# Kernel optimization log

Measured on AMD Instinct MI355X. Metric: run time of the kernel, lower is better.

Reference implementation:

```python
import jax, jax.numpy as jnp
import numpy as np

N, F_NODE, F_FLOW, H, E, B, L = 131072, 64, 16, 128, 2097152, 256, 32


def setup_inputs() -> dict:
    key = jax.random.key(0)
    ks = jax.random.split(key, 24)
    gn = lambda k, s, sc: jax.random.normal(k, s, jnp.float32) * sc
    s_in = 1.0 / np.sqrt(F_NODE)
    s_h = 1.0 / np.sqrt(H)
    s_f = 1.0 / np.sqrt(F_FLOW)
    s_c = 1.0 / np.sqrt(2 * H + H // 2)
    inp = {
        "x": gn(ks[0], (N, F_NODE), 1.0),
        "edge_index": jax.random.randint(ks[1], (2, E), 0, N),
        "batch": jnp.sort(jax.random.randint(ks[2], (N,), 0, B)),
        "path_idx": jax.random.randint(ks[3], (B, L), 0, N),
        "path_len": jax.random.randint(ks[4], (B,), 1, L + 1),
        "flow": gn(ks[5], (B, F_FLOW), 1.0),
        # SAGEConv1: out = mean_agg(x_j) @ Wl.T + b + x_i @ Wr.T
        "Wl1": gn(ks[6], (H, F_NODE), s_in), "Wr1": gn(ks[7], (H, F_NODE), s_in), "b1": gn(ks[8], (H,), s_in),
        "Wl2": gn(ks[9], (H, H), s_h), "Wr2": gn(ks[10], (H, H), s_h), "b2": gn(ks[11], (H,), s_h),
        # LSTM (torch gate order i,f,g,o)
        "Wih": gn(ks[12], (4 * H, H), s_h), "Whh": gn(ks[13], (4 * H, H), s_h),
        "bih": gn(ks[14], (4 * H,), s_h), "bhh": gn(ks[15], (4 * H,), s_h),
        # flow encoder Linear(F_FLOW, H//2)
        "Wf": gn(ks[16], (H // 2, F_FLOW), s_f), "bf": gn(ks[17], (H // 2,), s_f),
        # scorer MLP: Linear(2H+H//2, H) -> ReLU -> Linear(H, 1)
        "Ws1": gn(ks[18], (H, 2 * H + H // 2), s_c), "bs1": gn(ks[19], (H,), s_c),
        "Ws2": gn(ks[20], (1, H), s_h), "bs2": gn(ks[21], (1,), s_h),
    }
    return inp


def _sage(x, src, dst, Wl, Wr, b, n):
    agg = jax.ops.segment_sum(x[src], dst, num_segments=n)  # [n, d]
    cnt = jax.ops.segment_sum(jnp.ones((src.shape[0],), x.dtype), dst, num_segments=n)
    mean = agg / jnp.maximum(cnt, 1.0)[:, None]
    return mean @ Wl.T + b + x @ Wr.T


def _lstm_final_h(seq, valid, Wih, Whh, bih, bhh):
    # seq: [B, L, H], valid: [B, L] bool; returns h at each path's last valid step
    b, l, h = seq.shape
    h0 = jnp.zeros((b, h), seq.dtype)

    def step(carry, inp):
        hp, cp = carry
        x_t, v = inp  # [B,H], [B]
        gates = x_t @ Wih.T + hp @ Whh.T + bih + bhh
        i, f, g, o = jnp.split(gates, 4, axis=-1)
        c_new = jax.nn.sigmoid(f) * cp + jax.nn.sigmoid(i) * jnp.tanh(g)
        h_new = jax.nn.sigmoid(o) * jnp.tanh(c_new)
        m = v[:, None]
        return (jnp.where(m, h_new, hp), jnp.where(m, c_new, cp)), None

    (hf, _), _ = jax.lax.scan(step, (h0, h0),
                              (jnp.swapaxes(seq, 0, 1), jnp.swapaxes(valid, 0, 1)))
    return hf


def reference(x, edge_index, batch, path_idx, path_len, flow,
              Wl1, Wr1, b1, Wl2, Wr2, b2,
              Wih, Whh, bih, bhh, Wf, bf, Ws1, bs1, Ws2, bs2):
    n = x.shape[0]
    src, dst = edge_index[0], edge_index[1]
    h1 = jax.nn.relu(_sage(x, src, dst, Wl1, Wr1, b1, n))
    node_emb = jax.nn.relu(_sage(h1, src, dst, Wl2, Wr2, b2, n))

    # global mean pool per graph
    gsum = jax.ops.segment_sum(node_emb, batch, num_segments=B)
    gcnt = jax.ops.segment_sum(jnp.ones((n,), node_emb.dtype), batch, num_segments=B)
    graph_emb = gsum / jnp.maximum(gcnt, 1.0)[:, None]  # [B, H]

    flow_emb = jax.nn.relu(flow @ Wf.T + bf)  # [B, H//2]

    path_seq = node_emb[path_idx]  # [B, L, H]
    valid = jnp.arange(L)[None, :] < path_len[:, None]  # [B, L]
    path_emb = _lstm_final_h(path_seq, valid, Wih, Whh, bih, bhh)  # [B, H]

    combined = jnp.concatenate([graph_emb, path_emb, flow_emb], axis=-1)
    hidden = jax.nn.relu(combined @ Ws1.T + bs1)
    scores = hidden @ Ws2.T + bs2  # [B, 1]
    return scores[:, 0]  # matches torch.cat of per-path [1] outputs -> [B]
```

## Files before the change

### kernel.cpp

```cpp
#include <hip/hip_runtime.h>
#include <hip/hip_bf16.h>

#define N_NODES 131072
#define N_EDGES 2097152
#define BATCHES 256
#define LPATH   32
#define NB   256
#define NPB  512
#define GB   256
#define EPB  8192

typedef __hip_bfloat16 bf16;
using short8  = __attribute__((ext_vector_type(8))) short;
using floatx4 = __attribute__((ext_vector_type(4))) float;
using floatx2 = __attribute__((ext_vector_type(2))) float;

__device__ __forceinline__ float bl(unsigned u){ union {unsigned x; float f;} c; c.x = u << 16; return c.f; }
__device__ __forceinline__ float bh(unsigned u){ union {unsigned x; float f;} c; c.x = u & 0xffff0000u; return c.f; }
__device__ __forceinline__ unsigned packbf(float lo, float hi){
  bf16 l = __float2bfloat16(lo), h = __float2bfloat16(hi);
  unsigned short lu, hu;
  __builtin_memcpy(&lu, &l, 2); __builtin_memcpy(&hu, &h, 2);
  return (unsigned)lu | ((unsigned)hu << 16);
}
__device__ __forceinline__ float frcp(float x){ return __builtin_amdgcn_rcpf(x); }
__device__ __forceinline__ float sigf(float x){ return frcp(1.f + __expf(-x)); }
__device__ __forceinline__ float tanh_fast(float x){ return fmaf(2.f, frcp(1.f + __expf(-2.f * x)), -1.f); }

__global__ void mega0_k(const float* __restrict__ x, unsigned* __restrict__ xb8, bf16* __restrict__ Acat1,
                        const int* __restrict__ dst, int* __restrict__ cntA,
                        const float* __restrict__ Wl1, const float* __restrict__ Wr1,
                        const float* __restrict__ Wl2, const float* __restrict__ Wr2,
                        const float* __restrict__ Wih, const float* __restrict__ Whh,
                        const float* __restrict__ bih, const float* __restrict__ bhh,
                        bf16* __restrict__ Wcat1, bf16* __restrict__ Wcat2,
                        bf16* __restrict__ WihB, bf16* __restrict__ WhhB, float* __restrict__ bsumF,
                        const int* __restrict__ batch, int* __restrict__ starts){
  __shared__ int h[NB];
  int bid = blockIdx.x, tid = threadIdx.x;
  if (bid < 8192){
    int g = bid * 256 + tid;
    int n = g >> 4, p = g & 15;
    float4 v = *(const float4*)(x + (size_t)n * 64 + p * 4);
    uint2 wb; wb.x = packbf(v.x, v.y); wb.y = packbf(v.z, v.w);
    *(uint2*)(Acat1 + (size_t)n * 128 + 64 + p * 4) = wb;
    int w = 0;
    w = __builtin_amdgcn_cvt_pk_fp8_f32(v.x, v.y, w, false);
    w = __builtin_amdgcn_cvt_pk_fp8_f32(v.z, v.w, w, true);
    xb8[(size_t)n * 16 + p] = (unsigned)w;
  } else if (bid < 8448){
    int cb = bid - 8192;
    h[tid] = 0;
    __syncthreads();
    int base = cb * EPB;
    #pragma unroll
    for (int i = 0; i < EPB / 256; ++i){
      int d = dst[base + i * 256 + tid];
      atomicAdd(&h[d >> 9], 1);
    }
    __syncthreads();
    cntA[tid * GB + cb] = h[tid];
  } else if (bid < 9155){
    int g = (bid - 8448) * 256 + tid;
    if (g < 16384) {
      int hh = g >> 7, k = g & 127;
      float v = (k < 64) ? Wl1[hh * 64 + k] : Wr1[hh * 64 + (k - 64)];
      Wcat1[g] = __float2bfloat16(v);
    } else if (g < 49152) {
      int q = g - 16384;
      int hh = q >> 8, k = q & 255;
      float v = (k < 128) ? Wl2[hh * 128 + k] : Wr2[hh * 128 + (k - 128)];
      Wcat2[q] = __float2bfloat16(v);
    } else if (g < 114688) {
      int q = g - 49152;
      WihB[q] = __float2bfloat16(Wih[q]);
    } else if (g < 180224) {
      int q = g - 114688;
      WhhB[q] = __float2bfloat16(Whh[q]);
    } else if (g < 180736) {
      int k = g - 180224;
      bsumF[k] = bih[k] + bhh[k];
    }
  } else {
    int b = tid;
    int lo = 0, hi = N_NODES;
    while (lo < hi){ int mid = (lo + hi) >> 1; if (batch[mid] < b) lo = mid + 1; else hi = mid; }
    starts[b] = lo;
    if (b == 0) starts[BATCHES] = N_NODES;
  }
}

__global__ void scan1_k(const int* __restrict__ cnt, int* __restrict__ ofsA, int* __restrict__ bsum){
  __shared__ int sh[256];
  int t = threadIdx.x, i = blockIdx.x * 256 + t;
  int v = cnt[i];
  sh[t] = v; __syncthreads();
  int inc = v;
  for (int d = 1; d < 256; d <<= 1){
    int add = (t >= d) ? sh[t - d] : 0;
    __syncthreads();
    inc += add; sh[t] = inc;
    __syncthreads();
  }
  ofsA[i] = inc - v;
  if (t == 255) bsum[blockIdx.x] = inc;
}

__global__ void passA2_k(const int* __restrict__ src, const int* __restrict__ dst,
                         const int* __restrict__ ofsA, const int* __restrict__ bsum,
                         unsigned* __restrict__ ebuf){
  __shared__ int cur[NB];
  __shared__ int sc[NB];
  int tid = threadIdx.x;
  int v = bsum[tid];
  sc[tid] = v; __syncthreads();
  int inc = v;
  for (int d = 1; d < NB; d <<= 1){
    int add = (tid >= d) ? sc[tid - d] : 0;
    __syncthreads();
    inc += add; sc[tid] = inc;
    __syncthreads();
  }
  cur[tid] = ofsA[tid * GB + blockIdx.x] + (inc - v);
  __syncthreads();
  int base = blockIdx.x * EPB;
  #pragma unroll
  for (int i = 0; i < EPB / 256; ++i){
    int e = base + i * 256 + tid;
    int s = src[e], d = dst[e];
    int p = atomicAdd(&cur[d >> 9], 1);
    ebuf[p] = (unsigned)s | ((unsigned)(d & (NPB - 1)) << 17);
  }
}

__global__ void passB_k(const unsigned* __restrict__ ebuf, const int* __restrict__ bsum,
                        int* __restrict__ offs, int* __restrict__ srcS){
  __shared__ int ncnt[NPB];
  __shared__ int pairs[256];
  __shared__ int nofs[NPB];
  __shared__ int sc[NB];
  int k = blockIdx.x, tid = threadIdx.x;
  int v = bsum[tid];
  sc[tid] = v; __syncthreads();
  int inc0 = v;
  for (int d = 1; d < NB; d <<= 1){
    int add = (tid >= d) ? sc[tid - d] : 0;
    __syncthreads();
    inc0 += add; sc[tid] = inc0;
    __syncthreads();
  }
  sc[tid] = inc0 - v;
  __syncthreads();
  int bs = sc[k];
  int be = (k < NB - 1) ? sc[k + 1] : N_EDGES;
  ncnt[tid] = 0; ncnt[tid + 256] = 0;
  __syncthreads();
  for (int i = bs + tid; i < be; i += 256)
    atomicAdd(&ncnt[ebuf[i] >> 17], 1);
  __syncthreads();
  int p = ncnt[2 * tid] + ncnt[2 * tid + 1];
  pairs[tid] = p;
  __syncthreads();
  int inc = p;
  for (int d = 1; d < 256; d <<= 1){
    int add = (tid >= d) ? pairs[tid - d] : 0;
    __syncthreads();
    inc += add; pairs[tid] = inc;
    __syncthreads();
  }
  int ex = inc - p;
  nofs[2 * tid]     = ex;
  nofs[2 * tid + 1] = ex + ncnt[2 * tid];
  __syncthreads();
  offs[k * NPB + tid]       = bs + nofs[tid];
  offs[k * NPB + tid + 256] = bs + nofs[tid + 256];
  if (k == NB - 1 && tid == 0) offs[N_NODES] = N_EDGES;
  ncnt[tid] = nofs[tid]; ncnt[tid + 256] = nofs[tid + 256];
  __syncthreads();
  for (int i = bs + tid; i < be; i += 256){
    unsigned w = ebuf[i];
    int loc = w >> 17, sv = w & 0x1FFFF;
    int pp = atomicAdd(&ncnt[loc], 1);
    srcS[bs + pp] = sv;
  }
}

__global__ void agg1_k(const unsigned* __restrict__ xb8, const int* __restrict__ offs,
                       const int* __restrict__ srcS, bf16* __restrict__ Acat1){
  int wid = threadIdx.x >> 6, lane = threadIdx.x & 63;
  int n = blockIdx.x * 4 + wid;
  int s = offs[n], e = offs[n + 1];
  int slot = lane >> 3, fl = lane & 7;
  floatx2 a0={0,0}, a1={0,0}, a2={0,0}, a3={0,0};
  floatx2 c0={0,0}, c1={0,0}, c2={0,0}, c3={0,0};
  int i = s + slot;
  for (; i + 8 < e; i += 16){
    int sv0 = srcS[i], sv1 = srcS[i + 8];
    uint2 u = *(const uint2*)(xb8 + (size_t)sv0 * 16 + fl * 2);
    uint2 v = *(const uint2*)(xb8 + (size_t)sv1 * 16 + fl * 2);
    a0 += __builtin_amdgcn_cvt_pk_f32_fp8(u.x, false);
    a1 += __builtin_amdgcn_cvt_pk_f32_fp8(u.x, true);
    a2 += __builtin_amdgcn_cvt_pk_f32_fp8(u.y, false);
    a3 += __builtin_amdgcn_cvt_pk_f32_fp8(u.y, true);
    c0 += __builtin_amdgcn_cvt_pk_f32_fp8(v.x, false);
    c1 += __builtin_amdgcn_cvt_pk_f32_fp8(v.x, true);
    c2 += __builtin_amdgcn_cvt_pk_f32_fp8(v.y, false);
    c3 += __builtin_amdgcn_cvt_pk_f32_fp8(v.y, true);
  }
  if (i < e){
    int sv0 = srcS[i];
    uint2 u = *(const uint2*)(xb8 + (size_t)sv0 * 16 + fl * 2);
    a0 += __builtin_amdgcn_cvt_pk_f32_fp8(u.x, false);
    a1 += __builtin_amdgcn_cvt_pk_f32_fp8(u.x, true);
    a2 += __builtin_amdgcn_cvt_pk_f32_fp8(u.y, false);
    a3 += __builtin_amdgcn_cvt_pk_f32_fp8(u.y, true);
  }
  a0 += c0; a1 += c1; a2 += c2; a3 += c3;
  float f[8] = {a0.x, a0.y, a1.x, a1.y, a2.x, a2.y, a3.x, a3.y};
  #pragma unroll
  for (int j = 0; j < 8; ++j){
    f[j] += __shfl_xor(f[j], 8);
    f[j] += __shfl_xor(f[j], 16);
    f[j] += __shfl_xor(f[j], 32);
  }
  if (slot == 0){
    int d = e - s; if (d < 1) d = 1;
    float inv = 1.f / (float)d;
    uint4 w;
    w.x = packbf(f[0] * inv, f[1] * inv);
    w.y = packbf(f[2] * inv, f[3] * inv);
    w.z = packbf(f[4] * inv, f[5] * inv);
    w.w = packbf(f[6] * inv, f[7] * inv);
    *(uint4*)(Acat1 + (size_t)n * 128 + fl * 8) = w;
  }
}

__global__ void cvt8_k(const bf16* __restrict__ Acat2, unsigned* __restrict__ h1f8){
  int g = blockIdx.x * 256 + threadIdx.x;
  int n = g >> 5, p = g & 31;
  uint2 u = *(const uint2*)(Acat2 + (size_t)n * 256 + 128 + p * 4);
  int w = 0;
  w = __builtin_amdgcn_cvt_pk_fp8_f32(bl(u.x), bh(u.x), w, false);
  w = __builtin_amdgcn_cvt_pk_fp8_f32(bl(u.y), bh(u.y), w, true);
  h1f8[(size_t)n * 32 + p] = (unsigned)w;
}

__global__ void agg2_k(const int* __restrict__ offs, const int* __restrict__ srcS,
                       const unsigned* __restrict__ h1f8, bf16* __restrict__ Acat2){
  int wid = threadIdx.x >> 6, lane = threadIdx.x & 63;
  int n = blockIdx.x * 4 + wid;
  int s = offs[n], e = offs[n + 1];
  int slot = lane >> 4, fl = lane & 15;
  floatx2 a0={0,0}, a1={0,0}, a2={0,0}, a3={0,0};
  floatx2 b0={0,0}, b1={0,0}, b2={0,0}, b3={0,0};
  floatx2 c0={0,0}, c1={0,0}, c2={0,0}, c3={0,0};
  floatx2 d0={0,0}, d1={0,0}, d2={0,0}, d3={0,0};
  int i = s + slot;
  for (; i + 12 < e; i += 16){
    int sv0 = srcS[i], sv1 = srcS[i + 4], sv2 = srcS[i + 8], sv3 = srcS[i + 12];
    uint2 u = *(const uint2*)(h1f8 + (size_t)sv0 * 32 + fl * 2);
    uint2 v = *(const uint2*)(h1f8 + (size_t)sv1 * 32 + fl * 2);
    uint2 w = *(const uint2*)(h1f8 + (size_t)sv2 * 32 + fl * 2);
    uint2 z = *(const uint2*)(h1f8 + (size_t)sv3 * 32 + fl * 2);
    a0 += __builtin_amdgcn_cvt_pk_f32_fp8(u.x, false);
    a1 += __builtin_amdgcn_cvt_pk_f32_fp8(u.x, true);
    a2 += __builtin_amdgcn_cvt_pk_f32_fp8(u.y, false);
    a3 += __builtin_amdgcn_cvt_pk_f32_fp8(u.y, true);
    b0 += __builtin_amdgcn_cvt_pk_f32_fp8(v.x, false);
    b1 += __builtin_amdgcn_cvt_pk_f32_fp8(v.x, true);
    b2 += __builtin_amdgcn_cvt_pk_f32_fp8(v.y, false);
    b3 += __builtin_amdgcn_cvt_pk_f32_fp8(v.y, true);
    c0 += __builtin_amdgcn_cvt_pk_f32_fp8(w.x, false);
    c1 += __builtin_amdgcn_cvt_pk_f32_fp8(w.x, true);
    c2 += __builtin_amdgcn_cvt_pk_f32_fp8(w.y, false);
    c3 += __builtin_amdgcn_cvt_pk_f32_fp8(w.y, true);
    d0 += __builtin_amdgcn_cvt_pk_f32_fp8(z.x, false);
    d1 += __builtin_amdgcn_cvt_pk_f32_fp8(z.x, true);
    d2 += __builtin_amdgcn_cvt_pk_f32_fp8(z.y, false);
    d3 += __builtin_amdgcn_cvt_pk_f32_fp8(z.y, true);
  }
  for (; i < e; i += 4){
    int sv0 = srcS[i];
    uint2 u = *(const uint2*)(h1f8 + (size_t)sv0 * 32 + fl * 2);
    a0 += __builtin_amdgcn_cvt_pk_f32_fp8(u.x, false);
    a1 += __builtin_amdgcn_cvt_pk_f32_fp8(u.x, true);
    a2 += __builtin_amdgcn_cvt_pk_f32_fp8(u.y, false);
    a3 += __builtin_amdgcn_cvt_pk_f32_fp8(u.y, true);
  }
  a0 += b0; a1 += b1; a2 += b2; a3 += b3;
  c0 += d0; c1 += d1; c2 += d2; c3 += d3;
  a0 += c0; a1 += c1; a2 += c2; a3 += c3;
  float f[8] = {a0.x, a0.y, a1.x, a1.y, a2.x, a2.y, a3.x, a3.y};
  #pragma unroll
  for (int j = 0; j < 8; ++j){
    f[j] += __shfl_xor(f[j], 16);
    f[j] += __shfl_xor(f[j], 32);
  }
  if (slot == 0){
    int d = e - s; if (d < 1) d = 1;
    float inv = 1.f / (float)d;
    uint4 w;
    w.x = packbf(f[0] * inv, f[1] * inv);
    w.y = packbf(f[2] * inv, f[3] * inv);
    w.z = packbf(f[4] * inv, f[5] * inv);
    w.w = packbf(f[6] * inv, f[7] * inv);
    *(uint4*)(Acat2 + (size_t)n * 256 + fl * 8) = w;
  }
}

__global__ __launch_bounds__(256) void gemm_k(const bf16* __restrict__ A, int lda,
                                              const bf16* __restrict__ W, int K,
                                              const float* __restrict__ bias,
                                              void* __restrict__ out, int ldo, int outF32, int relu,
                                              const int* __restrict__ ridx){
  __shared__ bf16 Wl[128][136];
  int tid = threadIdx.x;
  int wid = tid >> 6, lane = tid & 63;
  int l16 = lane & 15, quad = lane >> 4;
  int rowBase  = blockIdx.x * 64 + wid * 16;
  int colGroup = blockIdx.y * 128;
  int arow = rowBase + l16;
  if (ridx) arow = ridx[arow];
  floatx4 acc[8] = {};
  int nStage = K >> 7;
  for (int ks = 0; ks < nStage; ++ks){
    __syncthreads();
    for (int c = tid; c < 2048; c += 256){
      int r = c >> 4, kc = (c & 15) << 3;
      *(uint4*)(&Wl[r][kc]) = *(const uint4*)(W + (size_t)(colGroup + r) * K + ks * 128 + kc);
    }
    __syncthreads();
    for (int kk = 0; kk < 4; ++kk){
      short8 af = *(const short8*)(A + (size_t)arow * lda + ks * 128 + kk * 32 + quad * 8);
      #pragma unroll
      for (int c = 0; c < 8; ++c){
        short8 bq = *(const short8*)(&Wl[c * 16 + l16][kk * 32 + quad * 8]);
        acc[c] = __builtin_amdgcn_mfma_f32_16x16x32_bf16(af, bq, acc[c], 0, 0, 0);
      }
    }
  }
  #pragma unroll
  for (int c = 0; c < 8; ++c){
    int col = colGroup + c * 16 + l16;
    float bv = bias ? bias[col] : 0.f;
    #pragma unroll
    for (int r = 0; r < 4; ++r){
      int row = rowBase + quad * 4 + r;
      float v = acc[c][r] + bv;
      if (relu) v = fmaxf(v, 0.f);
      if (outF32) ((float*)out)[(size_t)row * ldo + col] = v;
      else        ((bf16*)out)[(size_t)row * ldo + col]  = __float2bfloat16(v);
    }
  }
}

__global__ void poolflow_k(const bf16* __restrict__ ne, const int* __restrict__ starts,
                           const float* __restrict__ flow, const float* __restrict__ Wf,
                           const float* __restrict__ bfv, float* __restrict__ comb){
  __shared__ float sh[8][128];
  int bid = blockIdx.x;
  if (bid < 256){
    int b = bid;
    int q = threadIdx.x >> 6, lane = threadIdx.x & 63;
    int s = starts[b], e = starts[b + 1];
    float a0 = 0.f, a1 = 0.f;
    for (int i = s + q; i < e; i += 8){
      unsigned u = *(const unsigned*)(ne + (size_t)i * 128 + lane * 2);
      a0 += bl(u); a1 += bh(u);
    }
    sh[q][lane * 2] = a0; sh[q][lane * 2 + 1] = a1;
    __syncthreads();
    if (threadIdx.x < 128){
      int f = threadIdx.x;
      float tot = 0.f;
      #pragma unroll
      for (int k = 0; k < 8; ++k) tot += sh[k][f];
      int d = e - s; if (d < 1) d = 1;
      comb[b * 320 + f] = tot / (float)d;
    }
  } else {
    int g = (bid - 256) * 512 + threadIdx.x;
    int b = g >> 6, j = g & 63;
    float acc = bfv[j];
    for (int k = 0; k < 16; ++k)
      acc += flow[b * 16 + k] * Wf[j * 16 + k];
    comb[b * 320 + 256 + j] = fmaxf(acc, 0.f);
  }
}

__global__ __launch_bounds__(256, 1) void lstm_k(const bf16* __restrict__ Whh, const float* __restrict__ pre,
                                                 const int* __restrict__ path_len, float* __restrict__ comb){
  __shared__ bf16 hbuf[2][16][136];
  int tid = threadIdx.x;
  int w = tid >> 6, lane = tid & 63;
  int l16 = lane & 15, quad = lane >> 4;
  int b0 = blockIdx.x * 16;

  short8 wb[4][2][4];
  #pragma unroll
  for (int q = 0; q < 4; ++q)
    #pragma unroll
    for (int hf = 0; hf < 2; ++hf){
      const bf16* rp = Whh + (size_t)(q * 128 + w * 32 + hf * 16 + l16) * 128 + quad * 8;
      #pragma unroll
      for (int ks = 0; ks < 4; ++ks) wb[q][hf][ks] = *(const short8*)(rp + ks * 32);
    }

  int lenr[4];
  #pragma unroll
  for (int r = 0; r < 4; ++r){
    int L = path_len[b0 + quad * 4 + r];
    if (L < 1) L = 1; if (L > LPATH) L = LPATH;
    lenr[r] = L;
  }
  int maxlen = 1;
  for (int i = 0; i < 16; ++i){
    int L = path_len[b0 + i];
    if (L > LPATH) L = LPATH;
    if (L > maxlen) maxlen = L;
  }

  for (int i = tid; i < 1088; i += 256) ((unsigned*)&hbuf[0][0][0])[i] = 0;

  const float* pb[4];
  #pragma unroll
  for (int r = 0; r < 4; ++r)
    pb[r] = pre + (size_t)(b0 + quad * 4 + r) * LPATH * 512 + w * 32 + l16;

  float pv[4][2][4];
  #pragma unroll
  for (int q = 0; q < 4; ++q)
    #pragma unroll
    for (int hf = 0; hf < 2; ++hf)
      #pragma unroll
      for (int r = 0; r < 4; ++r)
        pv[q][hf][r] = pb[r][q * 128 + hf * 16];

  float cst[2][4] = {}, hst[2][4] = {};

  for (int t = 0; t < maxlen; ++t){
    int cur = t & 1, nxt = cur ^ 1;
    __syncthreads();
    short8 af[4];
    #pragma unroll
    for (int ks = 0; ks < 4; ++ks)
      af[ks] = *(const short8*)(&hbuf[cur][l16][ks * 32 + quad * 8]);
    int tn = (t + 1 < maxlen) ? t + 1 : t;
    float pnext[4][2][4];
    #pragma unroll
    for (int q = 0; q < 4; ++q)
      #pragma unroll
      for (int hf = 0; hf < 2; ++hf)
        #pragma unroll
        for (int r = 0; r < 4; ++r)
          pnext[q][hf][r] = pb[r][tn * 512 + q * 128 + hf * 16];
    floatx4 acc[4][2];
    #pragma unroll
    for (int q = 0; q < 4; ++q)
      #pragma unroll
      for (int hf = 0; hf < 2; ++hf){
        acc[q][hf][0] = pv[q][hf][0]; acc[q][hf][1] = pv[q][hf][1];
        acc[q][hf][2] = pv[q][hf][2]; acc[q][hf][3] = pv[q][hf][3];
      }
    #pragma unroll
    for (int ks = 0; ks < 4; ++ks)
      #pragma unroll
      for (int q = 0; q < 4; ++q)
        #pragma unroll
        for (int hf = 0; hf < 2; ++hf)
          acc[q][hf] = __builtin_amdgcn_mfma_f32_16x16x32_bf16(af[ks], wb[q][hf][ks], acc[q][hf], 0, 0, 0);
    #pragma unroll
    for (int hf = 0; hf < 2; ++hf)
      #pragma unroll
      for (int r = 0; r < 4; ++r){
        float ig = sigf(acc[0][hf][r]);
        float fg = sigf(acc[1][hf][r]);
        float gg = tanh_fast(acc[2][hf][r]);
        float og = sigf(acc[3][hf][r]);
        float cn = fmaf(fg, cst[hf][r], ig * gg);
        float hn = og * tanh_fast(cn);
        bool vld = t < lenr[r];
        cst[hf][r] = vld ? cn : cst[hf][r];
        hst[hf][r] = vld ? hn : hst[hf][r];
        hbuf[nxt][quad * 4 + r][w * 32 + hf * 16 + l16] = __float2bfloat16(hst[hf][r]);
      }
    #pragma unroll
    for (int q = 0; q < 4; ++q)
      #pragma unroll
      for (int hf = 0; hf < 2; ++hf)
        #pragma unroll
        for (int r = 0; r < 4; ++r)
          pv[q][hf][r] = pnext[q][hf][r];
  }

  #pragma unroll
  for (int hf = 0; hf < 2; ++hf)
    #pragma unroll
    for (int r = 0; r < 4; ++r)
      comb[(b0 + quad * 4 + r) * 320 + 128 + w * 32 + hf * 16 + l16] = hst[hf][r];
}

__global__ void head_k(const float* __restrict__ comb, const float* __restrict__ Ws1, const float* __restrict__ bs1,
                       const float* __restrict__ Ws2, const float* __restrict__ bs2, float* __restrict__ out){
  __shared__ float cl[320];
  __shared__ float red[128];
  int b = blockIdx.x, j = threadIdx.x;
  for (int k = j; k < 320; k += 128) cl[k] = comb[b * 320 + k];
  __syncthreads();
  float acc = bs1[j];
  const float4* wr = (const float4*)(Ws1 + (size_t)j * 320);
  #pragma unroll 4
  for (int kc = 0; kc < 80; ++kc){
    float4 u = wr[kc];
    int k = kc * 4;
    acc += u.x * cl[k] + u.y * cl[k + 1] + u.z * cl[k + 2] + u.w * cl[k + 3];
  }
  float hv = fmaxf(acc, 0.f);
  red[j] = hv * Ws2[j];
  __syncthreads();
  for (int s = 64; s > 0; s >>= 1){ if (j < s) red[j] += red[j + s]; __syncthreads(); }
  if (j == 0) out[b] = red[0] + bs2[0];
}

constexpr size_t OFF_OFFS   = 0;
constexpr size_t OFF_CNTA   = 524544;
constexpr size_t OFF_OFSA   = OFF_CNTA   + 262144;
constexpr size_t OFF_BSUM   = OFF_OFSA   + 262144;
constexpr size_t OFF_STARTS = OFF_BSUM   + 1024;
constexpr size_t OFF_SRCS   = OFF_STARTS + 2048;
constexpr size_t OFF_WCAT1  = OFF_SRCS   + 8388608;
constexpr size_t OFF_WCAT2  = OFF_WCAT1  + 32768;
constexpr size_t OFF_WIHB   = OFF_WCAT2  + 65536;
constexpr size_t OFF_WHHB   = OFF_WIHB   + 131072;
constexpr size_t OFF_BSUMF  = OFF_WHHB   + 131072;
constexpr size_t OFF_COMB   = OFF_BSUMF  + 2048;
constexpr size_t OFF_ACAT1  = OFF_COMB   + 327680;
constexpr size_t OFF_ACAT2  = OFF_ACAT1  + 33554432;
constexpr size_t OFF_H1F8   = OFF_ACAT1;
constexpr size_t OFF_EBUF   = OFF_ACAT2;
constexpr size_t OFF_PRE    = OFF_ACAT2  + 2097152;
constexpr size_t OFF_XB8    = OFF_ACAT2  + 50331648;

extern "C" void kernel_launch(void* const* d_in, const int* in_sizes, int n_in,
                              void* d_out, int out_size, void* d_ws, size_t ws_size,
                              hipStream_t stream){
  const float* x      = (const float*)d_in[0];
  const int* edge     = (const int*)d_in[1];
  const int* batch    = (const int*)d_in[2];
  const int* path_idx = (const int*)d_in[3];
  const int* path_len = (const int*)d_in[4];
  const float* flow   = (const float*)d_in[5];
  const float* Wl1 = (const float*)d_in[6];
  const float* Wr1 = (const float*)d_in[7];
  const float* b1  = (const float*)d_in[8];
  const float* Wl2 = (const float*)d_in[9];
  const float* Wr2 = (const float*)d_in[10];
  const float* b2  = (const float*)d_in[11];
  const float* Wih = (const float*)d_in[12];
  const float* Whh = (const float*)d_in[13];
  const float* bih = (const float*)d_in[14];
  const float* bhh = (const float*)d_in[15];
  const float* Wf  = (const float*)d_in[16];
  const float* bfv = (const float*)d_in[17];
  const float* Ws1 = (const float*)d_in[18];
  const float* bs1 = (const float*)d_in[19];
  const float* Ws2 = (const float*)d_in[20];
  const float* bs2 = (const float*)d_in[21];

  char* ws = (char*)d_ws;
  int* offs    = (int*)(ws + OFF_OFFS);
  int* cntA    = (int*)(ws + OFF_CNTA);
  int* ofsA    = (int*)(ws + OFF_OFSA);
  int* bsum    = (int*)(ws + OFF_BSUM);
  int* starts  = (int*)(ws + OFF_STARTS);
  int* srcS    = (int*)(ws + OFF_SRCS);
  bf16* Wcat1  = (bf16*)(ws + OFF_WCAT1);
  bf16* Wcat2  = (bf16*)(ws + OFF_WCAT2);
  bf16* WihB   = (bf16*)(ws + OFF_WIHB);
  bf16* WhhB   = (bf16*)(ws + OFF_WHHB);
  float* bsumF = (float*)(ws + OFF_BSUMF);
  float* comb  = (float*)(ws + OFF_COMB);
  bf16* Acat1  = (bf16*)(ws + OFF_ACAT1);
  bf16* node_emb = Acat1;
  bf16* Acat2  = (bf16*)(ws + OFF_ACAT2);
  unsigned* h1f8 = (unsigned*)(ws + OFF_H1F8);
  unsigned* ebuf = (unsigned*)(ws + OFF_EBUF);
  float* pre   = (float*)(ws + OFF_PRE);
  unsigned* xb8 = (unsigned*)(ws + OFF_XB8);

  mega0_k<<<9156, 256, 0, stream>>>(x, xb8, Acat1, edge + N_EDGES, cntA,
                                    Wl1, Wr1, Wl2, Wr2, Wih, Whh, bih, bhh,
                                    Wcat1, Wcat2, WihB, WhhB, bsumF, batch, starts);
  scan1_k<<<NB, 256, 0, stream>>>(cntA, ofsA, bsum);
  passA2_k<<<GB, 256, 0, stream>>>(edge, edge + N_EDGES, ofsA, bsum, ebuf);
  passB_k<<<NB, 256, 0, stream>>>(ebuf, bsum, offs, srcS);
  agg1_k<<<N_NODES / 4, 256, 0, stream>>>(xb8, offs, srcS, Acat1);
  gemm_k<<<dim3(N_NODES / 64, 1), 256, 0, stream>>>(Acat1, 128, Wcat1, 128, b1, Acat2 + 128, 256, 0, 1, nullptr);
  cvt8_k<<<N_NODES / 8, 256, 0, stream>>>(Acat2, h1f8);
  agg2_k<<<N_NODES / 4, 256, 0, stream>>>(offs, srcS, h1f8, Acat2);
  gemm_k<<<dim3(N_NODES / 64, 1), 256, 0, stream>>>(Acat2, 256, Wcat2, 256, b2, node_emb, 128, 0, 1, nullptr);
  poolflow_k<<<288, 512, 0, stream>>>(node_emb, starts, flow, Wf, bfv, comb);
  gemm_k<<<dim3(BATCHES * LPATH / 64, 4), 256, 0, stream>>>(node_emb, 128, WihB, 128, bsumF, pre, 512, 1, 0, path_idx);
  lstm_k<<<BATCHES / 16, 256, 0, stream>>>(WhhB, pre, path_len, comb);
  head_k<<<BATCHES, 128, 0, stream>>>(comb, Ws1, bs1, Ws2, bs2, (float*)d_out);
}
```

Before: 438.7 us.

## Fuse fp8 conversion into layer-1 GEMM, split concat buffers, merge tail kernels

The layer-1 GEMM now writes bf16 h1 to its own buffer and, in the same epilogue, builds an fp8 copy through shared memory. This removes the separate cvt8 pass. The layer-2 GEMM reads the mean and h1 from two separate 128-wide buffers instead of one 256-wide concatenated buffer. The path-gather input GEMM, the graph pooling and the flow encoder are merged into one launch, and agg2 unrolls its edge loop less to use fewer registers. The cost is more specialised kernels, extra workspace aliasing and less memory-level parallelism in agg2.

```diff
diff --git a/kernel.cpp b/kernel.cpp
--- a/kernel.cpp
+++ b/kernel.cpp
@@ -235,51 +235,73 @@
   }
 }
 
-__global__ void cvt8_k(const bf16* __restrict__ Acat2, unsigned* __restrict__ h1f8){
-  int g = blockIdx.x * 256 + threadIdx.x;
-  int n = g >> 5, p = g & 31;
-  uint2 u = *(const uint2*)(Acat2 + (size_t)n * 256 + 128 + p * 4);
-  int w = 0;
-  w = __builtin_amdgcn_cvt_pk_fp8_f32(bl(u.x), bh(u.x), w, false);
-  w = __builtin_amdgcn_cvt_pk_fp8_f32(bl(u.y), bh(u.y), w, true);
-  h1f8[(size_t)n * 32 + p] = (unsigned)w;
+__global__ __launch_bounds__(256) void gemmf8_k(const bf16* __restrict__ A, const bf16* __restrict__ W,
+                                                const float* __restrict__ bias,
+                                                bf16* __restrict__ h1B, unsigned* __restrict__ h1f8){
+  __shared__ bf16 Wl[128][136];
+  __shared__ unsigned char f8t[64][144];
+  int tid = threadIdx.x;
+  int wid = tid >> 6, lane = tid & 63;
+  int l16 = lane & 15, quad = lane >> 4;
+  int rowBase = blockIdx.x * 64 + wid * 16;
+  floatx4 acc[8] = {};
+  for (int c = tid; c < 2048; c += 256){
+    int r = c >> 4, kc = (c & 15) << 3;
+    *(uint4*)(&Wl[r][kc]) = *(const uint4*)(W + (size_t)r * 128 + kc);
+  }
+  __syncthreads();
+  for (int kk = 0; kk < 4; ++kk){
+    short8 af = *(const short8*)(A + (size_t)(rowBase + l16) * 128 + kk * 32 + quad * 8);
+    #pragma unroll
+    for (int c = 0; c < 8; ++c){
+      short8 bq = *(const short8*)(&Wl[c * 16 + l16][kk * 32 + quad * 8]);
+      acc[c] = __builtin_amdgcn_mfma_f32_16x16x32_bf16(af, bq, acc[c], 0, 0, 0);
+    }
+  }
+  #pragma unroll
+  for (int c = 0; c < 8; ++c){
+    int col = c * 16 + l16;
+    float bv = bias[col];
+    #pragma unroll
+    for (int r = 0; r < 4; ++r){
+      int rl = wid * 16 + quad * 4 + r;
+      float v = fmaxf(acc[c][r] + bv, 0.f);
+      h1B[(size_t)(blockIdx.x * 64 + rl) * 128 + col] = __float2bfloat16(v);
+      unsigned pk = (unsigned)__builtin_amdgcn_cvt_pk_fp8_f32(v, v, 0, false);
+      f8t[rl][col] = (unsigned char)(pk & 0xFF);
+    }
+  }
+  __syncthreads();
+  for (int it = tid; it < 512; it += 256){
+    int row = it >> 3, seg = it & 7;
+    uint4 val = *(const uint4*)(&f8t[row][seg * 16]);
+    *(uint4*)((char*)h1f8 + (size_t)(blockIdx.x * 64 + row) * 128 + seg * 16) = val;
+  }
 }
 
 __global__ void agg2_k(const int* __restrict__ offs, const int* __restrict__ srcS,
-                       const unsigned* __restrict__ h1f8, bf16* __restrict__ Acat2){
+                       const unsigned* __restrict__ h1f8, bf16* __restrict__ meanB){
   int wid = threadIdx.x >> 6, lane = threadIdx.x & 63;
   int n = blockIdx.x * 4 + wid;
   int s = offs[n], e = offs[n + 1];
   int slot = lane >> 4, fl = lane & 15;
   floatx2 a0={0,0}, a1={0,0}, a2={0,0}, a3={0,0};
-  floatx2 b0={0,0}, b1={0,0}, b2={0,0}, b3={0,0};
   floatx2 c0={0,0}, c1={0,0}, c2={0,0}, c3={0,0};
-  floatx2 d0={0,0}, d1={0,0}, d2={0,0}, d3={0,0};
   int i = s + slot;
-  for (; i + 12 < e; i += 16){
-    int sv0 = srcS[i], sv1 = srcS[i + 4], sv2 = srcS[i + 8], sv3 = srcS[i + 12];
+  for (; i + 4 < e; i += 8){
+    int sv0 = srcS[i], sv1 = srcS[i + 4];
     uint2 u = *(const uint2*)(h1f8 + (size_t)sv0 * 32 + fl * 2);
     uint2 v = *(const uint2*)(h1f8 + (size_t)sv1 * 32 + fl * 2);
-    uint2 w = *(const uint2*)(h1f8 + (size_t)sv2 * 32 + fl * 2);
-    uint2 z = *(const uint2*)(h1f8 + (size_t)sv3 * 32 + fl * 2);
     a0 += __builtin_amdgcn_cvt_pk_f32_fp8(u.x, false);
     a1 += __builtin_amdgcn_cvt_pk_f32_fp8(u.x, true);
     a2 += __builtin_amdgcn_cvt_pk_f32_fp8(u.y, false);
     a3 += __builtin_amdgcn_cvt_pk_f32_fp8(u.y, true);
-    b0 += __builtin_amdgcn_cvt_pk_f32_fp8(v.x, false);
-    b1 += __builtin_amdgcn_cvt_pk_f32_fp8(v.x, true);
-    b2 += __builtin_amdgcn_cvt_pk_f32_fp8(v.y, false);
-    b3 += __builtin_amdgcn_cvt_pk_f32_fp8(v.y, true);
-    c0 += __builtin_amdgcn_cvt_pk_f32_fp8(w.x, false);
-    c1 += __builtin_amdgcn_cvt_pk_f32_fp8(w.x, true);
-    c2 += __builtin_amdgcn_cvt_pk_f32_fp8(w.y, false);
-    c3 += __builtin_amdgcn_cvt_pk_f32_fp8(w.y, true);
-    d0 += __builtin_amdgcn_cvt_pk_f32_fp8(z.x, false);
-    d1 += __builtin_amdgcn_cvt_pk_f32_fp8(z.x, true);
-    d2 += __builtin_amdgcn_cvt_pk_f32_fp8(z.y, false);
-    d3 += __builtin_amdgcn_cvt_pk_f32_fp8(z.y, true);
-  }
-  for (; i < e; i += 4){
+    c0 += __builtin_amdgcn_cvt_pk_f32_fp8(v.x, false);
+    c1 += __builtin_amdgcn_cvt_pk_f32_fp8(v.x, true);
+    c2 += __builtin_amdgcn_cvt_pk_f32_fp8(v.y, false);
+    c3 += __builtin_amdgcn_cvt_pk_f32_fp8(v.y, true);
+  }
+  if (i < e){
     int sv0 = srcS[i];
     uint2 u = *(const uint2*)(h1f8 + (size_t)sv0 * 32 + fl * 2);
     a0 += __builtin_amdgcn_cvt_pk_f32_fp8(u.x, false);
@@ -287,8 +309,6 @@
     a2 += __builtin_amdgcn_cvt_pk_f32_fp8(u.y, false);
     a3 += __builtin_amdgcn_cvt_pk_f32_fp8(u.y, true);
   }
-  a0 += b0; a1 += b1; a2 += b2; a3 += b3;
-  c0 += d0; c1 += d1; c2 += d2; c3 += d3;
   a0 += c0; a1 += c1; a2 += c2; a3 += c3;
   float f[8] = {a0.x, a0.y, a1.x, a1.y, a2.x, a2.y, a3.x, a3.y};
   #pragma unroll
@@ -304,34 +324,30 @@
     w.y = packbf(f[2] * inv, f[3] * inv);
     w.z = packbf(f[4] * inv, f[5] * inv);
     w.w = packbf(f[6] * inv, f[7] * inv);
-    *(uint4*)(Acat2 + (size_t)n * 256 + fl * 8) = w;
-  }
-}
-
-__global__ __launch_bounds__(256) void gemm_k(const bf16* __restrict__ A, int lda,
-                                              const bf16* __restrict__ W, int K,
-                                              const float* __restrict__ bias,
-                                              void* __restrict__ out, int ldo, int outF32, int relu,
-                                              const int* __restrict__ ridx){
+    *(uint4*)(meanB + (size_t)n * 128 + fl * 8) = w;
+  }
+}
+
+__global__ __launch_bounds__(256) void gemm2sp_k(const bf16* __restrict__ A0, const bf16* __restrict__ A1,
+                                                 const bf16* __restrict__ W, const float* __restrict__ bias,
+                                                 bf16* __restrict__ out){
   __shared__ bf16 Wl[128][136];
   int tid = threadIdx.x;
   int wid = tid >> 6, lane = tid & 63;
   int l16 = lane & 15, quad = lane >> 4;
-  int rowBase  = blockIdx.x * 64 + wid * 16;
-  int colGroup = blockIdx.y * 128;
-  int arow = rowBase + l16;
-  if (ridx) arow = ridx[arow];
+  int rowBase = blockIdx.x * 64 + wid * 16;
   floatx4 acc[8] = {};
-  int nStage = K >> 7;
-  for (int ks = 0; ks < nStage; ++ks){
+  #pragma unroll
+  for (int ks = 0; ks < 2; ++ks){
     __syncthreads();
     for (int c = tid; c < 2048; c += 256){
       int r = c >> 4, kc = (c & 15) << 3;
-      *(uint4*)(&Wl[r][kc]) = *(const uint4*)(W + (size_t)(colGroup + r) * K + ks * 128 + kc);
-    }
-    __syncthreads();
+      *(uint4*)(&Wl[r][kc]) = *(const uint4*)(W + (size_t)r * 256 + ks * 128 + kc);
+    }
+    __syncthreads();
+    const bf16* Ab = ks ? A1 : A0;
     for (int kk = 0; kk < 4; ++kk){
-      short8 af = *(const short8*)(A + (size_t)arow * lda + ks * 128 + kk * 32 + quad * 8);
+      short8 af = *(const short8*)(Ab + (size_t)(rowBase + l16) * 128 + kk * 32 + quad * 8);
       #pragma unroll
       for (int c = 0; c < 8; ++c){
         short8 bq = *(const short8*)(&Wl[c * 16 + l16][kk * 32 + quad * 8]);
@@ -341,45 +357,75 @@
   }
   #pragma unroll
   for (int c = 0; c < 8; ++c){
-    int col = colGroup + c * 16 + l16;
-    float bv = bias ? bias[col] : 0.f;
+    int col = c * 16 + l16;
+    float bv = bias[col];
     #pragma unroll
     for (int r = 0; r < 4; ++r){
       int row = rowBase + quad * 4 + r;
-      float v = acc[c][r] + bv;
-      if (relu) v = fmaxf(v, 0.f);
-      if (outF32) ((float*)out)[(size_t)row * ldo + col] = v;
-      else        ((bf16*)out)[(size_t)row * ldo + col]  = __float2bfloat16(v);
-    }
-  }
-}
-
-__global__ void poolflow_k(const bf16* __restrict__ ne, const int* __restrict__ starts,
-                           const float* __restrict__ flow, const float* __restrict__ Wf,
-                           const float* __restrict__ bfv, float* __restrict__ comb){
-  __shared__ float sh[8][128];
-  int bid = blockIdx.x;
-  if (bid < 256){
-    int b = bid;
-    int q = threadIdx.x >> 6, lane = threadIdx.x & 63;
+      out[(size_t)row * 128 + col] = __float2bfloat16(fmaxf(acc[c][r] + bv, 0.f));
+    }
+  }
+}
+
+__global__ __launch_bounds__(256) void tail0_k(const bf16* __restrict__ ne, const bf16* __restrict__ W,
+                                               const float* __restrict__ bias, float* __restrict__ pre,
+                                               const int* __restrict__ ridx,
+                                               const int* __restrict__ starts,
+                                               const float* __restrict__ flow, const float* __restrict__ Wf,
+                                               const float* __restrict__ bfv, float* __restrict__ comb){
+  __shared__ bf16 Wl[128][136];
+  __shared__ float sh[4][128];
+  int bid = blockIdx.x, tid = threadIdx.x;
+  if (bid < 512){
+    int bx = bid >> 2, by = bid & 3;
+    int wid = tid >> 6, lane = tid & 63;
+    int l16 = lane & 15, quad = lane >> 4;
+    int rowBase = bx * 64 + wid * 16;
+    int colGroup = by * 128;
+    int arow = ridx[rowBase + l16];
+    floatx4 acc[8] = {};
+    for (int c = tid; c < 2048; c += 256){
+      int r = c >> 4, kc = (c & 15) << 3;
+      *(uint4*)(&Wl[r][kc]) = *(const uint4*)(W + (size_t)(colGroup + r) * 128 + kc);
+    }
+    __syncthreads();
+    for (int kk = 0; kk < 4; ++kk){
+      short8 af = *(const short8*)(ne + (size_t)arow * 128 + kk * 32 + quad * 8);
+      #pragma unroll
+      for (int c = 0; c < 8; ++c){
+        short8 bq = *(const short8*)(&Wl[c * 16 + l16][kk * 32 + quad * 8]);
+        acc[c] = __builtin_amdgcn_mfma_f32_16x16x32_bf16(af, bq, acc[c], 0, 0, 0);
+      }
+    }
+    #pragma unroll
+    for (int c = 0; c < 8; ++c){
+      int col = colGroup + c * 16 + l16;
+      float bv = bias[col];
+      #pragma unroll
+      for (int r = 0; r < 4; ++r){
+        int row = rowBase + quad * 4 + r;
+        pre[(size_t)row * 512 + col] = acc[c][r] + bv;
+      }
+    }
+  } else if (bid < 768){
+    int b = bid - 512;
+    int q = tid >> 6, lane = tid & 63;
     int s = starts[b], e = starts[b + 1];
     float a0 = 0.f, a1 = 0.f;
-    for (int i = s + q; i < e; i += 8){
+    for (int i = s + q; i < e; i += 4){
       unsigned u = *(const unsigned*)(ne + (size_t)i * 128 + lane * 2);
       a0 += bl(u); a1 += bh(u);
     }
     sh[q][lane * 2] = a0; sh[q][lane * 2 + 1] = a1;
     __syncthreads();
-    if (threadIdx.x < 128){
-      int f = threadIdx.x;
-      float tot = 0.f;
-      #pragma unroll
-      for (int k = 0; k < 8; ++k) tot += sh[k][f];
+    if (tid < 128){
+      int f = tid;
+      float tot = sh[0][f] + sh[1][f] + sh[2][f] + sh[3][f];
       int d = e - s; if (d < 1) d = 1;
       comb[b * 320 + f] = tot / (float)d;
     }
   } else {
-    int g = (bid - 256) * 512 + threadIdx.x;
+    int g = (bid - 768) * 256 + tid;
     int b = g >> 6, j = g & 63;
     float acc = bfv[j];
     for (int k = 0; k < 16; ++k)
@@ -534,12 +580,14 @@
 constexpr size_t OFF_WHHB   = OFF_WIHB   + 131072;
 constexpr size_t OFF_BSUMF  = OFF_WHHB   + 131072;
 constexpr size_t OFF_COMB   = OFF_BSUMF  + 2048;
-constexpr size_t OFF_ACAT1  = OFF_COMB   + 327680;
-constexpr size_t OFF_ACAT2  = OFF_ACAT1  + 33554432;
-constexpr size_t OFF_H1F8   = OFF_ACAT1;
-constexpr size_t OFF_EBUF   = OFF_ACAT2;
-constexpr size_t OFF_PRE    = OFF_ACAT2  + 2097152;
-constexpr size_t OFF_XB8    = OFF_ACAT2  + 50331648;
+constexpr size_t OFF_R1     = OFF_COMB   + 327680;
+constexpr size_t OFF_R2     = OFF_R1     + 33554432;
+constexpr size_t OFF_EBUF   = OFF_R2;
+constexpr size_t OFF_H1B    = OFF_R2;
+constexpr size_t OFF_PRE    = OFF_R2;
+constexpr size_t OFF_XB8    = OFF_R2 + 33554432;
+constexpr size_t OFF_H1F8   = OFF_R2 + 33554432;
+constexpr size_t OFF_NE     = OFF_R2 + 33554432;
 
 extern "C" void kernel_launch(void* const* d_in, const int* in_sizes, int n_in,
                               void* d_out, int out_size, void* d_ws, size_t ws_size,
@@ -580,13 +628,14 @@
   bf16* WhhB   = (bf16*)(ws + OFF_WHHB);
   float* bsumF = (float*)(ws + OFF_BSUMF);
   float* comb  = (float*)(ws + OFF_COMB);
-  bf16* Acat1  = (bf16*)(ws + OFF_ACAT1);
-  bf16* node_emb = Acat1;
-  bf16* Acat2  = (bf16*)(ws + OFF_ACAT2);
+  bf16* Acat1  = (bf16*)(ws + OFF_R1);
+  bf16* meanB  = (bf16*)(ws + OFF_R1);
+  unsigned* ebuf = (unsigned*)(ws + OFF_EBUF);
+  bf16* h1B    = (bf16*)(ws + OFF_H1B);
+  float* pre   = (float*)(ws + OFF_PRE);
+  unsigned* xb8  = (unsigned*)(ws + OFF_XB8);
   unsigned* h1f8 = (unsigned*)(ws + OFF_H1F8);
-  unsigned* ebuf = (unsigned*)(ws + OFF_EBUF);
-  float* pre   = (float*)(ws + OFF_PRE);
-  unsigned* xb8 = (unsigned*)(ws + OFF_XB8);
+  bf16* node_emb = (bf16*)(ws + OFF_NE);
 
   mega0_k<<<9156, 256, 0, stream>>>(x, xb8, Acat1, edge + N_EDGES, cntA,
                                     Wl1, Wr1, Wl2, Wr2, Wih, Whh, bih, bhh,
@@ -595,12 +644,10 @@
   passA2_k<<<GB, 256, 0, stream>>>(edge, edge + N_EDGES, ofsA, bsum, ebuf);
   passB_k<<<NB, 256, 0, stream>>>(ebuf, bsum, offs, srcS);
   agg1_k<<<N_NODES / 4, 256, 0, stream>>>(xb8, offs, srcS, Acat1);
-  gemm_k<<<dim3(N_NODES / 64, 1), 256, 0, stream>>>(Acat1, 128, Wcat1, 128, b1, Acat2 + 128, 256, 0, 1, nullptr);
-  cvt8_k<<<N_NODES / 8, 256, 0, stream>>>(Acat2, h1f8);
-  agg2_k<<<N_NODES / 4, 256, 0, stream>>>(offs, srcS, h1f8, Acat2);
-  gemm_k<<<dim3(N_NODES / 64, 1), 256, 0, stream>>>(Acat2, 256, Wcat2, 256, b2, node_emb, 128, 0, 1, nullptr);
-  poolflow_k<<<288, 512, 0, stream>>>(node_emb, starts, flow, Wf, bfv, comb);
-  gemm_k<<<dim3(BATCHES * LPATH / 64, 4), 256, 0, stream>>>(node_emb, 128, WihB, 128, bsumF, pre, 512, 1, 0, path_idx);
+  gemmf8_k<<<N_NODES / 64, 256, 0, stream>>>(Acat1, Wcat1, b1, h1B, h1f8);
+  agg2_k<<<N_NODES / 4, 256, 0, stream>>>(offs, srcS, h1f8, meanB);
+  gemm2sp_k<<<N_NODES / 64, 256, 0, stream>>>(meanB, h1B, Wcat2, b2, node_emb);
+  tail0_k<<<832, 256, 0, stream>>>(node_emb, WihB, bsumF, pre, path_idx, starts, flow, Wf, bfv, comb);
   lstm_k<<<BATCHES / 16, 256, 0, stream>>>(WhhB, pre, path_len, comb);
   head_k<<<BATCHES, 128, 0, stream>>>(comb, Ws1, bs1, Ws2, bs2, (float*)d_out);
 }
```

Result: faster. 424.7 us (-3.2%).
